# Optimization experiments

Hardware: AMD Instinct MI355X
Metric: run time of the kernel (lower is better)

## Reference

```python
import jax, jax.numpy as jnp
import numpy as np

D, FF, E, K = 1024, 1024, 8, 2  # d_model, ffn_dim, n_experts, top_k
B, S = 4, 1024


def _gelu(x):
    # torch F.gelu default is the exact erf form
    return jax.nn.gelu(x, approximate=False)


def setup_inputs() -> dict:
    key = jax.random.key(0)
    ks = jax.random.split(key, 12)
    s = 0.02
    return {
        "x": jax.random.normal(ks[0], (B, S, D), jnp.float32),
        "gate_w": jax.random.normal(ks[1], (D, E), jnp.float32) * s,
        "gate_b": jnp.zeros((E,), jnp.float32),
        # shared expert (n_shared = 1)
        "sw1": jax.random.normal(ks[2], (D, FF), jnp.float32) * s,
        "sb1": jnp.zeros((FF,), jnp.float32),
        "sw2": jax.random.normal(ks[3], (FF, D), jnp.float32) * s,
        "sb2": jnp.zeros((D,), jnp.float32),
        # routed experts, stacked over E
        "w1": jax.random.normal(ks[4], (E, D, FF), jnp.float32) * s,
        "b1": jnp.zeros((E, FF), jnp.float32),
        "w2": jax.random.normal(ks[5], (E, FF, D), jnp.float32) * s,
        "b2": jnp.zeros((E, D), jnp.float32),
    }


def reference(x, gate_w, gate_b, sw1, sb1, sw2, sb2, w1, b1, w2, b2):
    Bb, Ss, Dm = x.shape
    t = x.reshape(-1, Dm)  # [T, D]
    T = t.shape[0]

    # shared expert(s)
    shared = _gelu(t @ sw1 + sb1) @ sw2 + sb2  # [T, D]

    # gating: softmax over experts, then top-k
    probs = jax.nn.softmax(t @ gate_w + gate_b, axis=-1)  # [T, E]
    topk_p, topk_i = jax.lax.top_k(probs, K)  # [T, K]

    # combine weights: sparse [T, E] with top-k probs (top_k indices are distinct)
    combine = jnp.zeros((T, E), t.dtype).at[
        jnp.arange(T)[:, None], topk_i
    ].set(topk_p)

    # expert FFNs computed densely, combined with sparse routing weights;
    # mathematically identical to the masked gather-GEMM-scatter loop
    h = _gelu(jnp.einsum("td,edf->etf", t, w1) + b1[:, None, :])  # [E, T, FF]
    y = jnp.einsum("etf,efd->etd", h, w2) + b2[:, None, :]        # [E, T, D]
    routed = jnp.einsum("te,etd->td", combine, y)                  # [T, D]

    return (routed + shared).reshape(Bb, Ss, Dm)
```

## Files before the change

### kernel.cpp

```cpp
#include <hip/hip_runtime.h>
#include <hip/hip_bf16.h>


typedef short short8 __attribute__((ext_vector_type(8)));
typedef float f32x4  __attribute__((ext_vector_type(4)));

#define T_TOK 4096
#define NSLOT 8192
#define NWG   832
#define CHUNK 104

#define OFF_XB    (size_t)0
#define OFF_W1T   (size_t)8388608
#define OFF_W2T   (size_t)25165824
#define OFF_SW1T  (size_t)41943040
#define OFF_SW2T  (size_t)44040192
#define OFF_HS    (size_t)46137344
#define OFF_HR    (size_t)54525952
#define OFF_META  (size_t)73400320
#define OFF_ROWMAP (size_t)73400576
#define OFF_ROWW  (size_t)73437440
#define OFF_TKI   (size_t)73474304
#define OFF_TKP   (size_t)73507072

__device__ __forceinline__ unsigned short f2bf(float f) {
  __hip_bfloat16 h = __float2bfloat16(f);
  return __builtin_bit_cast(unsigned short, h);
}
__device__ __forceinline__ float gelu_exact(float x) {
  return 0.5f * x * (1.0f + erff(x * 0.70710678118654752f));
}

#define GLOAD16(g, l)                                                          \
  __builtin_amdgcn_global_load_lds(                                            \
      (const __attribute__((address_space(1))) void*)(g),                      \
      (__attribute__((address_space(3))) void*)(l), 16, 0, 0)


__global__ void k_transpose(const float* __restrict__ w1, const float* __restrict__ w2,
                            const float* __restrict__ sw1, const float* __restrict__ sw2,
                            unsigned short* __restrict__ w1t, unsigned short* __restrict__ w2t,
                            unsigned short* __restrict__ sw1t, unsigned short* __restrict__ sw2t) {
  __shared__ float tile[32][33];
  int z = blockIdx.z;
  const float* src; unsigned short* dst;
  if (z < 8)       { src = w1 + (size_t)z * 1048576;        dst = w1t + (size_t)z * 1048576; }
  else if (z < 16) { src = w2 + (size_t)(z - 8) * 1048576;  dst = w2t + (size_t)(z - 8) * 1048576; }
  else if (z == 16){ src = sw1; dst = sw1t; }
  else             { src = sw2; dst = sw2t; }
  int tx = threadIdx.x, ty = threadIdx.y;
  int gx = blockIdx.x * 32 + tx;
#pragma unroll
  for (int j = 0; j < 4; j++) {
    int gy = blockIdx.y * 32 + ty + j * 8;
    tile[ty + j * 8][tx] = src[(size_t)gy * 1024 + gx];
  }
  __syncthreads();
#pragma unroll
  for (int j = 0; j < 4; j++) {
    int orow = blockIdx.x * 32 + ty + j * 8;
    int ocol = blockIdx.y * 32 + tx;
    dst[(size_t)orow * 1024 + ocol] = f2bf(tile[tx][ty + j * 8]);
  }
}

__global__ void k_gate(const float* __restrict__ x, const float* __restrict__ gw,
                       const float* __restrict__ gb, int* __restrict__ tki,
                       float* __restrict__ tkp, unsigned short* __restrict__ xb) {
  int wv = threadIdx.x >> 6, l = threadIdx.x & 63;
  int t = blockIdx.x * 4 + wv;
  float acc[8] = {0, 0, 0, 0, 0, 0, 0, 0};
  const float* xr = x + (size_t)t * 1024;
  unsigned short* xbr = xb + (size_t)t * 1024;
#pragma unroll
  for (int j = 0; j < 16; j++) {
    int k = j * 64 + l;
    float xv = xr[k];
    xbr[k] = f2bf(xv);
    const float4* g4 = (const float4*)(gw + (size_t)k * 8);
    float4 ga = g4[0], gbv = g4[1];
    acc[0] += xv * ga.x; acc[1] += xv * ga.y; acc[2] += xv * ga.z; acc[3] += xv * ga.w;
    acc[4] += xv * gbv.x; acc[5] += xv * gbv.y; acc[6] += xv * gbv.z; acc[7] += xv * gbv.w;
  }
#pragma unroll
  for (int off = 32; off > 0; off >>= 1) {
#pragma unroll
    for (int e = 0; e < 8; e++) acc[e] += __shfl_xor(acc[e], off);
  }
  if (l == 0) {
    float lg[8], p[8];
    float m = -1e30f;
#pragma unroll
    for (int e = 0; e < 8; e++) { lg[e] = acc[e] + gb[e]; m = fmaxf(m, lg[e]); }
    float s = 0.f;
#pragma unroll
    for (int e = 0; e < 8; e++) { p[e] = expf(lg[e] - m); s += p[e]; }
    float inv = 1.0f / s;
#pragma unroll
    for (int e = 0; e < 8; e++) p[e] *= inv;
    int i0 = 0;
#pragma unroll
    for (int e = 1; e < 8; e++) if (p[e] > p[i0]) i0 = e;
    int i1 = (i0 == 0) ? 1 : 0;
#pragma unroll
    for (int e = 0; e < 8; e++) if (e != i0 && p[e] > p[i1]) i1 = e;
    tki[t * 2] = i0; tki[t * 2 + 1] = i1;
    tkp[t * 2] = p[i0]; tkp[t * 2 + 1] = p[i1];
  }
}

__global__ void k_route(const int* __restrict__ tki, const float* __restrict__ tkp,
                        int* __restrict__ counts, int* __restrict__ basev,
                        int* __restrict__ rowmap, float* __restrict__ roww) {
  int e = blockIdx.x, tid = threadIdx.x;
  int lane = tid & 63, wv = tid >> 6;
  int c[8] = {0, 0, 0, 0, 0, 0, 0, 0};
  for (int i = tid; i < NSLOT; i += 256) {
    int v = tki[i];
#pragma unroll
    for (int q = 0; q < 8; q++) c[q] += (v == q);
  }
  __shared__ int red[8][64];
#pragma unroll
  for (int q = 0; q < 8; q++) {
#pragma unroll
    for (int off = 32; off > 0; off >>= 1) c[q] += __shfl_xor(c[q], off);
  }
  if (lane == 0) {
#pragma unroll
    for (int q = 0; q < 8; q++) red[q][wv] = c[q];
  }
  __syncthreads();
  __shared__ int cnt_s[8], base_s[8];
  if (tid == 0) {
    int off = 0;
#pragma unroll
    for (int q = 0; q < 8; q++) {
      int cq = red[q][0] + red[q][1] + red[q][2] + red[q][3];
      cnt_s[q] = cq; base_s[q] = off;
      off += (cq + 127) & ~127;
    }
    counts[e] = cnt_s[e];
    basev[e] = base_s[e];
  }
  __syncthreads();
  __shared__ int warpsum[4];
  int wpos = base_s[e];
  for (int i0 = 0; i0 < NSLOT; i0 += 256) {
    int i = i0 + tid;
    bool pred = (tki[i] == e);
    unsigned long long mask = __ballot(pred);
    int wpre = __popcll(mask & ((1ull << lane) - 1));
    if (lane == 0) warpsum[wv] = __popcll(mask);
    __syncthreads();
    int wbase = 0;
    for (int w = 0; w < wv; w++) wbase += warpsum[w];
    int total = warpsum[0] + warpsum[1] + warpsum[2] + warpsum[3];
    if (pred) {
      int pos = wpos + wbase + wpre;
      rowmap[pos] = i >> 1;
      roww[pos] = tkp[i];
    }
    wpos += total;
    __syncthreads();
  }
}

#define STAGE_TILE(buf, kk0)                                                   \
  {                                                                            \
    _Pragma("unroll") for (int i = 0; i < 4; i++) {                            \
      int q = i * 4 + wave;                                                    \
      int c = q * 64 + lane;                                                   \
      int m = c >> 3, s = c & 7;                                               \
      int ks = s ^ (m & 7);                                                    \
      GLOAD16(Amat + arow[i] * 1024 + (kk0) + ks * 8, &ldsA[buf][q * 512]);    \
    }                                                                          \
    _Pragma("unroll") for (int i = 0; i < 4; i++) {                            \
      int q = i * 4 + wave;                                                    \
      int c = q * 64 + lane;                                                   \
      int n = c >> 3, s = c & 7;                                               \
      int ks = s ^ (n & 7);                                                    \
      GLOAD16(Bmat + (size_t)(n0 + n) * 1024 + (kk0) + ks * 8,                 \
              &ldsB[buf][q * 512]);                                            \
    }                                                                          \
  }

template <int PHASE>
__global__ __launch_bounds__(256, 2) void k_ffn(
    const unsigned short* __restrict__ As,
    const unsigned short* __restrict__ Ar,
    const unsigned short* __restrict__ Bsh, const float* __restrict__ bsh,
    const unsigned short* __restrict__ Brt, const float* __restrict__ brt,
    unsigned short* __restrict__ Hsh, unsigned short* __restrict__ Hrt,
    float* __restrict__ outf,
    const int* __restrict__ rowmap, const float* __restrict__ roww,
    const int* __restrict__ counts, const int* __restrict__ bases) {
  __shared__ unsigned short ldsA[2][128 * 64];
  __shared__ unsigned short ldsB[2][128 * 64];

  int bid = blockIdx.x;
  int j = (bid & 7) * CHUNK + (bid >> 3);
  int z = -1, rel = j;
  if (rel < 256) {
    z = 0;
  } else {
    rel -= 256;
#pragma unroll
    for (int e = 0; e < 8; e++) {
      int nye = ((counts[e] + 127) >> 7) << 3;
      if (z < 0) {
        if (rel < nye) z = e + 1; else rel -= nye;
      }
    }
    if (z < 0) return;
  }
  int row0 = (rel >> 3) * 128;
  int n0 = (rel & 7) * 128;

  int nrows, rbase = 0;
  const unsigned short* Bmat; const float* bvec; const unsigned short* Amat;
  if (z == 0) {
    nrows = T_TOK; Bmat = Bsh; bvec = bsh; Amat = As;
  } else {
    int e = z - 1;
    nrows = counts[e]; rbase = bases[e];
    Bmat = Brt + (size_t)e * 1048576;
    bvec = brt + (size_t)e * 1024;
    Amat = (PHASE == 1) ? As : Ar;
  }
  int tid = threadIdx.x, wave = tid >> 6, lane = tid & 63;
  int wm = wave >> 1, wn = wave & 1;

  long arow[4];
#pragma unroll
  for (int i = 0; i < 4; i++) {
    int q = i * 4 + wave;
    int m = (q * 64 + lane) >> 3;
    int r = row0 + m;
    if (r >= nrows) r = nrows - 1;
    if (z == 0)            arow[i] = r;
    else if (PHASE == 1)   arow[i] = rowmap[rbase + r];
    else                   arow[i] = rbase + r;
  }

  f32x4 acc[4][4];
#pragma unroll
  for (int i = 0; i < 4; i++)
#pragma unroll
    for (int j2 = 0; j2 < 4; j2++) acc[i][j2] = (f32x4){0.f, 0.f, 0.f, 0.f};

  STAGE_TILE(0, 0);

  for (int t = 0; t < 16; ++t) {
    int b = t & 1;
    if (t < 15) {
      STAGE_TILE(b ^ 1, (t + 1) * 64);
      asm volatile("s_waitcnt vmcnt(8)" ::: "memory");
    } else {
      asm volatile("s_waitcnt vmcnt(0)" ::: "memory");
    }
    __builtin_amdgcn_s_barrier();
#pragma unroll
    for (int kk = 0; kk < 2; kk++) {
      short8 af[4], bfr[4];
      int kc0 = kk * 4 + (lane >> 4);
#pragma unroll
      for (int fi = 0; fi < 4; fi++) {
        int m = wm * 64 + fi * 16 + (lane & 15);
        int slot = kc0 ^ (m & 7);
        af[fi] = *(const short8*)&ldsA[b][m * 64 + slot * 8];
      }
#pragma unroll
      for (int fj = 0; fj < 4; fj++) {
        int n = wn * 64 + fj * 16 + (lane & 15);
        int slot = kc0 ^ (n & 7);
        bfr[fj] = *(const short8*)&ldsB[b][n * 64 + slot * 8];
      }
#pragma unroll
      for (int fi = 0; fi < 4; fi++)
#pragma unroll
        for (int fj = 0; fj < 4; fj++)
          acc[fi][fj] = __builtin_amdgcn_mfma_f32_16x16x32_bf16(af[fi], bfr[fj], acc[fi][fj], 0, 0, 0);
    }
    __builtin_amdgcn_s_barrier();
  }

#pragma unroll
  for (int fi = 0; fi < 4; fi++) {
#pragma unroll
    for (int rg = 0; rg < 4; rg++) {
      int lr = wm * 64 + fi * 16 + (lane >> 4) * 4 + rg;
      int r = row0 + lr;
      if (r >= nrows) continue;
      if (PHASE == 1) {
        unsigned short* dst = (z == 0) ? (Hsh + (size_t)r * 1024)
                                       : (Hrt + (size_t)(rbase + r) * 1024);
#pragma unroll
        for (int fj = 0; fj < 4; fj++) {
          int col = n0 + wn * 64 + fj * 16 + (lane & 15);
          dst[col] = f2bf(gelu_exact(acc[fi][fj][rg] + bvec[col]));
        }
      } else {
        if (z == 0) {
#pragma unroll
          for (int fj = 0; fj < 4; fj++) {
            int col = n0 + wn * 64 + fj * 16 + (lane & 15);
            atomicAdd(&outf[(size_t)r * 1024 + col], acc[fi][fj][rg] + bvec[col]);
          }
        } else {
          int tok = rowmap[rbase + r];
          float p = roww[rbase + r];
#pragma unroll
          for (int fj = 0; fj < 4; fj++) {
            int col = n0 + wn * 64 + fj * 16 + (lane & 15);
            atomicAdd(&outf[(size_t)tok * 1024 + col], p * (acc[fi][fj][rg] + bvec[col]));
          }
        }
      }
    }
  }
}

extern "C" void kernel_launch(void* const* d_in, const int* in_sizes, int n_in,
                              void* d_out, int out_size, void* d_ws, size_t ws_size,
                              hipStream_t stream) {
  const float* x   = (const float*)d_in[0];
  const float* gw  = (const float*)d_in[1];
  const float* gb  = (const float*)d_in[2];
  const float* sw1 = (const float*)d_in[3];
  const float* sb1 = (const float*)d_in[4];
  const float* sw2 = (const float*)d_in[5];
  const float* sb2 = (const float*)d_in[6];
  const float* w1  = (const float*)d_in[7];
  const float* b1  = (const float*)d_in[8];
  const float* w2  = (const float*)d_in[9];
  const float* b2  = (const float*)d_in[10];
  float* out = (float*)d_out;
  char* ws = (char*)d_ws;

  unsigned short* xb   = (unsigned short*)(ws + OFF_XB);
  unsigned short* w1t  = (unsigned short*)(ws + OFF_W1T);
  unsigned short* w2t  = (unsigned short*)(ws + OFF_W2T);
  unsigned short* sw1t = (unsigned short*)(ws + OFF_SW1T);
  unsigned short* sw2t = (unsigned short*)(ws + OFF_SW2T);
  unsigned short* Hs   = (unsigned short*)(ws + OFF_HS);
  unsigned short* Hr   = (unsigned short*)(ws + OFF_HR);
  int*   counts = (int*)(ws + OFF_META);
  int*   basev  = counts + 8;
  int*   rowmap = (int*)(ws + OFF_ROWMAP);
  float* roww   = (float*)(ws + OFF_ROWW);
  int*   tki    = (int*)(ws + OFF_TKI);
  float* tkp    = (float*)(ws + OFF_TKP);

  hipMemsetAsync(out, 0, (size_t)out_size * sizeof(float), stream);
  k_transpose<<<dim3(32, 32, 18), dim3(32, 8), 0, stream>>>(w1, w2, sw1, sw2, w1t, w2t, sw1t, sw2t);
  k_gate<<<1024, 256, 0, stream>>>(x, gw, gb, tki, tkp, xb);
  k_route<<<8, 256, 0, stream>>>(tki, tkp, counts, basev, rowmap, roww);

  k_ffn<1><<<NWG, 256, 0, stream>>>(xb, xb, sw1t, sb1, w1t, b1, Hs, Hr,
                                    nullptr, rowmap, roww, counts, basev);
  k_ffn<2><<<NWG, 256, 0, stream>>>(Hs, Hr, sw2t, sb2, w2t, b2, nullptr, nullptr,
                                    out, rowmap, roww, counts, basev);
}
```

Before: 214.8 us.

## Load MFMA fragments directly from global memory instead of staging through LDS

Removes the double-buffered LDS staging (global_load_lds, swizzle, barriers) and has each wave load its A and B MFMA fragments straight from global memory in a fully unrolled K loop. This eliminates LDS traffic and block-wide barriers. In exchange, operands shared between waves are no longer reused through LDS, so each tile is fetched several times from L2/global, and the loads are 16-byte strided accesses per lane. Latency hiding now relies on the compiler scheduling the unrolled loads.

```diff
diff --git a/kernel.cpp b/kernel.cpp
--- a/kernel.cpp
+++ b/kernel.cpp
@@ -30,11 +30,6 @@
 __device__ __forceinline__ float gelu_exact(float x) {
   return 0.5f * x * (1.0f + erff(x * 0.70710678118654752f));
 }
-
-#define GLOAD16(g, l)                                                          \
-  __builtin_amdgcn_global_load_lds(                                            \
-      (const __attribute__((address_space(1))) void*)(g),                      \
-      (__attribute__((address_space(3))) void*)(l), 16, 0, 0)
 
 
 __global__ void k_transpose(const float* __restrict__ w1, const float* __restrict__ w2,
@@ -166,25 +161,6 @@
   }
 }
 
-#define STAGE_TILE(buf, kk0)                                                   \
-  {                                                                            \
-    _Pragma("unroll") for (int i = 0; i < 4; i++) {                            \
-      int q = i * 4 + wave;                                                    \
-      int c = q * 64 + lane;                                                   \
-      int m = c >> 3, s = c & 7;                                               \
-      int ks = s ^ (m & 7);                                                    \
-      GLOAD16(Amat + arow[i] * 1024 + (kk0) + ks * 8, &ldsA[buf][q * 512]);    \
-    }                                                                          \
-    _Pragma("unroll") for (int i = 0; i < 4; i++) {                            \
-      int q = i * 4 + wave;                                                    \
-      int c = q * 64 + lane;                                                   \
-      int n = c >> 3, s = c & 7;                                               \
-      int ks = s ^ (n & 7);                                                    \
-      GLOAD16(Bmat + (size_t)(n0 + n) * 1024 + (kk0) + ks * 8,                 \
-              &ldsB[buf][q * 512]);                                            \
-    }                                                                          \
-  }
-
 template <int PHASE>
 __global__ __launch_bounds__(256, 2) void k_ffn(
     const unsigned short* __restrict__ As,
@@ -195,9 +171,6 @@
     float* __restrict__ outf,
     const int* __restrict__ rowmap, const float* __restrict__ roww,
     const int* __restrict__ counts, const int* __restrict__ bases) {
-  __shared__ unsigned short ldsA[2][128 * 64];
-  __shared__ unsigned short ldsB[2][128 * 64];
-
   int bid = blockIdx.x;
   int j = (bid & 7) * CHUNK + (bid >> 3);
   int z = -1, rel = j;
@@ -230,17 +203,24 @@
   }
   int tid = threadIdx.x, wave = tid >> 6, lane = tid & 63;
   int wm = wave >> 1, wn = wave & 1;
-
-  long arow[4];
-#pragma unroll
-  for (int i = 0; i < 4; i++) {
-    int q = i * 4 + wave;
-    int m = (q * 64 + lane) >> 3;
-    int r = row0 + m;
+  int l15 = lane & 15, lh = lane >> 4;
+
+  const unsigned short* aptr[4];
+  const unsigned short* bptr[4];
+#pragma unroll
+  for (int fi = 0; fi < 4; fi++) {
+    int r = row0 + wm * 64 + fi * 16 + l15;
     if (r >= nrows) r = nrows - 1;
-    if (z == 0)            arow[i] = r;
-    else if (PHASE == 1)   arow[i] = rowmap[rbase + r];
-    else                   arow[i] = rbase + r;
+    long rg;
+    if (z == 0)          rg = r;
+    else if (PHASE == 1) rg = rowmap[rbase + r];
+    else                 rg = rbase + r;
+    aptr[fi] = Amat + rg * 1024 + lh * 8;
+  }
+#pragma unroll
+  for (int fj = 0; fj < 4; fj++) {
+    int n = n0 + wn * 64 + fj * 16 + l15;
+    bptr[fj] = Bmat + (size_t)n * 1024 + lh * 8;
   }
 
   f32x4 acc[4][4];
@@ -249,47 +229,25 @@
 #pragma unroll
     for (int j2 = 0; j2 < 4; j2++) acc[i][j2] = (f32x4){0.f, 0.f, 0.f, 0.f};
 
-  STAGE_TILE(0, 0);
-
-  for (int t = 0; t < 16; ++t) {
-    int b = t & 1;
-    if (t < 15) {
-      STAGE_TILE(b ^ 1, (t + 1) * 64);
-      asm volatile("s_waitcnt vmcnt(8)" ::: "memory");
-    } else {
-      asm volatile("s_waitcnt vmcnt(0)" ::: "memory");
-    }
-    __builtin_amdgcn_s_barrier();
-#pragma unroll
-    for (int kk = 0; kk < 2; kk++) {
-      short8 af[4], bfr[4];
-      int kc0 = kk * 4 + (lane >> 4);
-#pragma unroll
-      for (int fi = 0; fi < 4; fi++) {
-        int m = wm * 64 + fi * 16 + (lane & 15);
-        int slot = kc0 ^ (m & 7);
-        af[fi] = *(const short8*)&ldsA[b][m * 64 + slot * 8];
-      }
-#pragma unroll
-      for (int fj = 0; fj < 4; fj++) {
-        int n = wn * 64 + fj * 16 + (lane & 15);
-        int slot = kc0 ^ (n & 7);
-        bfr[fj] = *(const short8*)&ldsB[b][n * 64 + slot * 8];
-      }
-#pragma unroll
-      for (int fi = 0; fi < 4; fi++)
-#pragma unroll
-        for (int fj = 0; fj < 4; fj++)
-          acc[fi][fj] = __builtin_amdgcn_mfma_f32_16x16x32_bf16(af[fi], bfr[fj], acc[fi][fj], 0, 0, 0);
-    }
-    __builtin_amdgcn_s_barrier();
+#pragma unroll
+  for (int c = 0; c < 32; ++c) {
+    short8 af[4], bfr[4];
+#pragma unroll
+    for (int fi = 0; fi < 4; fi++) af[fi] = *(const short8*)(aptr[fi] + c * 32);
+#pragma unroll
+    for (int fj = 0; fj < 4; fj++) bfr[fj] = *(const short8*)(bptr[fj] + c * 32);
+#pragma unroll
+    for (int fi = 0; fi < 4; fi++)
+#pragma unroll
+      for (int fj = 0; fj < 4; fj++)
+        acc[fi][fj] = __builtin_amdgcn_mfma_f32_16x16x32_bf16(af[fi], bfr[fj], acc[fi][fj], 0, 0, 0);
   }
 
 #pragma unroll
   for (int fi = 0; fi < 4; fi++) {
 #pragma unroll
     for (int rg = 0; rg < 4; rg++) {
-      int lr = wm * 64 + fi * 16 + (lane >> 4) * 4 + rg;
+      int lr = wm * 64 + fi * 16 + lh * 4 + rg;
       int r = row0 + lr;
       if (r >= nrows) continue;
       if (PHASE == 1) {
@@ -297,14 +255,14 @@
                                        : (Hrt + (size_t)(rbase + r) * 1024);
 #pragma unroll
         for (int fj = 0; fj < 4; fj++) {
-          int col = n0 + wn * 64 + fj * 16 + (lane & 15);
+          int col = n0 + wn * 64 + fj * 16 + l15;
           dst[col] = f2bf(gelu_exact(acc[fi][fj][rg] + bvec[col]));
         }
       } else {
         if (z == 0) {
 #pragma unroll
           for (int fj = 0; fj < 4; fj++) {
-            int col = n0 + wn * 64 + fj * 16 + (lane & 15);
+            int col = n0 + wn * 64 + fj * 16 + l15;
             atomicAdd(&outf[(size_t)r * 1024 + col], acc[fi][fj][rg] + bvec[col]);
           }
         } else {
@@ -312,7 +270,7 @@
           float p = roww[rbase + r];
 #pragma unroll
           for (int fj = 0; fj < 4; fj++) {
-            int col = n0 + wn * 64 + fj * 16 + (lane & 15);
+            int col = n0 + wn * 64 + fj * 16 + l15;
             atomicAdd(&outf[(size_t)tok * 1024 + col], p * (acc[fi][fj][rg] + bvec[col]));
           }
         }
```

New measurement: 349.4 us. 62.6% more time.

## Enlarge FFN GEMM tiles to 256x256 with 512-thread workgroups

Applied to the files above, without the earlier changes.

Raises the FFN GEMM tile from 128x128 to 256x256 with 8 waves per workgroup, each wave computing a 128x64 sub-tile (8x4 MFMA fragments). The grid shrinks from 832 to 224 workgroups and load addresses are precomputed per thread, with an early exit for empty expert row tiles. The aim is more reuse per byte of global and LDS traffic. In exchange it uses 128KB of LDS and twice the accumulator registers, which may limit occupancy, and it wastes more work on partially filled expert tiles.

```diff
diff --git a/kernel.cpp b/kernel.cpp
--- a/kernel.cpp
+++ b/kernel.cpp
@@ -7,8 +7,8 @@
 
 #define T_TOK 4096
 #define NSLOT 8192
-#define NWG   832
-#define CHUNK 104
+#define NWG   224
+#define CHUNK 28
 
 #define OFF_XB    (size_t)0
 #define OFF_W1T   (size_t)8388608
@@ -168,25 +168,15 @@
 
 #define STAGE_TILE(buf, kk0)                                                   \
   {                                                                            \
-    _Pragma("unroll") for (int i = 0; i < 4; i++) {                            \
-      int q = i * 4 + wave;                                                    \
-      int c = q * 64 + lane;                                                   \
-      int m = c >> 3, s = c & 7;                                               \
-      int ks = s ^ (m & 7);                                                    \
-      GLOAD16(Amat + arow[i] * 1024 + (kk0) + ks * 8, &ldsA[buf][q * 512]);    \
-    }                                                                          \
-    _Pragma("unroll") for (int i = 0; i < 4; i++) {                            \
-      int q = i * 4 + wave;                                                    \
-      int c = q * 64 + lane;                                                   \
-      int n = c >> 3, s = c & 7;                                               \
-      int ks = s ^ (n & 7);                                                    \
-      GLOAD16(Bmat + (size_t)(n0 + n) * 1024 + (kk0) + ks * 8,                 \
-              &ldsB[buf][q * 512]);                                            \
-    }                                                                          \
+    _Pragma("unroll") for (int i = 0; i < 4; i++)                              \
+      GLOAD16(Amat + arow[i] * 1024 + (kk0) + aks[i],                          \
+              &ldsA[buf][(i * 8 + wave) * 512]);                               \
+    _Pragma("unroll") for (int i = 0; i < 4; i++)                              \
+      GLOAD16(Bmat + bof[i] + (kk0), &ldsB[buf][(i * 8 + wave) * 512]);        \
   }
 
 template <int PHASE>
-__global__ __launch_bounds__(256, 2) void k_ffn(
+__global__ __launch_bounds__(512, 2) void k_ffn(
     const unsigned short* __restrict__ As,
     const unsigned short* __restrict__ Ar,
     const unsigned short* __restrict__ Bsh, const float* __restrict__ bsh,
@@ -195,27 +185,27 @@
     float* __restrict__ outf,
     const int* __restrict__ rowmap, const float* __restrict__ roww,
     const int* __restrict__ counts, const int* __restrict__ bases) {
-  __shared__ unsigned short ldsA[2][128 * 64];
-  __shared__ unsigned short ldsB[2][128 * 64];
+  __shared__ unsigned short ldsA[2][256 * 64];
+  __shared__ unsigned short ldsB[2][256 * 64];
 
   int bid = blockIdx.x;
   int j = (bid & 7) * CHUNK + (bid >> 3);
   int z = -1, rel = j;
-  if (rel < 256) {
+  if (rel < 64) {
     z = 0;
   } else {
-    rel -= 256;
+    rel -= 64;
 #pragma unroll
     for (int e = 0; e < 8; e++) {
-      int nye = ((counts[e] + 127) >> 7) << 3;
+      int nye = ((counts[e] + 255) >> 8) << 2;
       if (z < 0) {
         if (rel < nye) z = e + 1; else rel -= nye;
       }
     }
     if (z < 0) return;
   }
-  int row0 = (rel >> 3) * 128;
-  int n0 = (rel & 7) * 128;
+  int row0 = (rel >> 2) * 256;
+  int n0 = (rel & 3) * 256;
 
   int nrows, rbase = 0;
   const unsigned short* Bmat; const float* bvec; const unsigned short* Amat;
@@ -224,18 +214,22 @@
   } else {
     int e = z - 1;
     nrows = counts[e]; rbase = bases[e];
+    if (row0 >= nrows) return;
     Bmat = Brt + (size_t)e * 1048576;
     bvec = brt + (size_t)e * 1024;
     Amat = (PHASE == 1) ? As : Ar;
   }
   int tid = threadIdx.x, wave = tid >> 6, lane = tid & 63;
-  int wm = wave >> 1, wn = wave & 1;
-
-  long arow[4];
+  int wm = wave >> 2, wn = wave & 3;
+  int l15 = lane & 15, lh = lane >> 4;
+
+  long arow[4]; int aks[4]; size_t bof[4];
 #pragma unroll
   for (int i = 0; i < 4; i++) {
-    int q = i * 4 + wave;
-    int m = (q * 64 + lane) >> 3;
+    int c = (i * 8 + wave) * 64 + lane;
+    int m = c >> 3, s = c & 7;
+    aks[i] = (s ^ (m & 7)) * 8;
+    bof[i] = (size_t)(n0 + m) * 1024 + aks[i];
     int r = row0 + m;
     if (r >= nrows) r = nrows - 1;
     if (z == 0)            arow[i] = r;
@@ -243,9 +237,9 @@
     else                   arow[i] = rbase + r;
   }
 
-  f32x4 acc[4][4];
-#pragma unroll
-  for (int i = 0; i < 4; i++)
+  f32x4 acc[8][4];
+#pragma unroll
+  for (int i = 0; i < 8; i++)
 #pragma unroll
     for (int j2 = 0; j2 < 4; j2++) acc[i][j2] = (f32x4){0.f, 0.f, 0.f, 0.f};
 
@@ -262,22 +256,22 @@
     __builtin_amdgcn_s_barrier();
 #pragma unroll
     for (int kk = 0; kk < 2; kk++) {
-      short8 af[4], bfr[4];
-      int kc0 = kk * 4 + (lane >> 4);
-#pragma unroll
-      for (int fi = 0; fi < 4; fi++) {
-        int m = wm * 64 + fi * 16 + (lane & 15);
+      short8 af[8], bfr[4];
+      int kc0 = kk * 4 + lh;
+#pragma unroll
+      for (int fi = 0; fi < 8; fi++) {
+        int m = wm * 128 + fi * 16 + l15;
         int slot = kc0 ^ (m & 7);
         af[fi] = *(const short8*)&ldsA[b][m * 64 + slot * 8];
       }
 #pragma unroll
       for (int fj = 0; fj < 4; fj++) {
-        int n = wn * 64 + fj * 16 + (lane & 15);
+        int n = wn * 64 + fj * 16 + l15;
         int slot = kc0 ^ (n & 7);
         bfr[fj] = *(const short8*)&ldsB[b][n * 64 + slot * 8];
       }
 #pragma unroll
-      for (int fi = 0; fi < 4; fi++)
+      for (int fi = 0; fi < 8; fi++)
 #pragma unroll
         for (int fj = 0; fj < 4; fj++)
           acc[fi][fj] = __builtin_amdgcn_mfma_f32_16x16x32_bf16(af[fi], bfr[fj], acc[fi][fj], 0, 0, 0);
@@ -286,10 +280,10 @@
   }
 
 #pragma unroll
-  for (int fi = 0; fi < 4; fi++) {
+  for (int fi = 0; fi < 8; fi++) {
 #pragma unroll
     for (int rg = 0; rg < 4; rg++) {
-      int lr = wm * 64 + fi * 16 + (lane >> 4) * 4 + rg;
+      int lr = wm * 128 + fi * 16 + lh * 4 + rg;
       int r = row0 + lr;
       if (r >= nrows) continue;
       if (PHASE == 1) {
@@ -297,14 +291,14 @@
                                        : (Hrt + (size_t)(rbase + r) * 1024);
 #pragma unroll
         for (int fj = 0; fj < 4; fj++) {
-          int col = n0 + wn * 64 + fj * 16 + (lane & 15);
+          int col = n0 + wn * 64 + fj * 16 + l15;
           dst[col] = f2bf(gelu_exact(acc[fi][fj][rg] + bvec[col]));
         }
       } else {
         if (z == 0) {
 #pragma unroll
           for (int fj = 0; fj < 4; fj++) {
-            int col = n0 + wn * 64 + fj * 16 + (lane & 15);
+            int col = n0 + wn * 64 + fj * 16 + l15;
             atomicAdd(&outf[(size_t)r * 1024 + col], acc[fi][fj][rg] + bvec[col]);
           }
         } else {
@@ -312,7 +306,7 @@
           float p = roww[rbase + r];
 #pragma unroll
           for (int fj = 0; fj < 4; fj++) {
-            int col = n0 + wn * 64 + fj * 16 + (lane & 15);
+            int col = n0 + wn * 64 + fj * 16 + l15;
             atomicAdd(&outf[(size_t)tok * 1024 + col], p * (acc[fi][fj][rg] + bvec[col]));
           }
         }
@@ -357,8 +351,8 @@
   k_gate<<<1024, 256, 0, stream>>>(x, gw, gb, tki, tkp, xb);
   k_route<<<8, 256, 0, stream>>>(tki, tkp, counts, basev, rowmap, roww);
 
-  k_ffn<1><<<NWG, 256, 0, stream>>>(xb, xb, sw1t, sb1, w1t, b1, Hs, Hr,
+  k_ffn<1><<<NWG, 512, 0, stream>>>(xb, xb, sw1t, sb1, w1t, b1, Hs, Hr,
                                     nullptr, rowmap, roww, counts, basev);
-  k_ffn<2><<<NWG, 256, 0, stream>>>(Hs, Hr, sw2t, sb2, w2t, b2, nullptr, nullptr,
+  k_ffn<2><<<NWG, 512, 0, stream>>>(Hs, Hr, sw2t, sb2, w2t, b2, nullptr, nullptr,
                                     out, rowmap, roww, counts, basev);
 }
```

Measured after the change: 207.2 us. 3.5% less time.
